# Optimization experiments

Measured on AMD Instinct MI355X. Metric: run time of the kernel, lower is better.

Reference implementation:

```python
import jax, jax.numpy as jnp
import numpy as np
import math

B, L, D = 4, 4096, 1024
PI = math.pi
LN_EPS = 1e-5


def setup_inputs() -> dict:
    key = jax.random.key(0)
    ks = jax.random.split(key, 16)
    s = 1.0 / math.sqrt(D)
    inp = {
        "x": jax.random.normal(ks[0], (B, L, D), dtype=jnp.float32),
        # Linear weights stored as [in, out] (torch W.T)
        "Wk": jax.random.normal(ks[1], (D, D), dtype=jnp.float32) * s,
        "bk": jnp.zeros((D,), dtype=jnp.float32),
        "Wq": jax.random.normal(ks[2], (D, D), dtype=jnp.float32) * s,
        "bq": jnp.zeros((D,), dtype=jnp.float32),
        "Wv": jax.random.normal(ks[3], (D, D), dtype=jnp.float32) * s,
        "bv": jnp.zeros((D,), dtype=jnp.float32),
        "ln_g": jnp.ones((D,), dtype=jnp.float32),
        "ln_b": jnp.zeros((D,), dtype=jnp.float32),
        "Wo": jax.random.normal(ks[4], (D, D), dtype=jnp.float32) * s,
        "bo": jnp.zeros((D,), dtype=jnp.float32),
        "Wg1": jax.random.normal(ks[5], (D, D // 4), dtype=jnp.float32) * s,
        "bg1": jnp.zeros((D // 4,), dtype=jnp.float32),
        "Wg2": jax.random.normal(ks[6], (D // 4, 1), dtype=jnp.float32) * (2.0 / math.sqrt(D)),
        "bg2": jnp.zeros((1,), dtype=jnp.float32),
        "pos_phases": jax.random.normal(ks[7], (L, D), dtype=jnp.float32) * PI,
    }
    return inp


def _layernorm(x, g, b):
    mu = jnp.mean(x, axis=-1, keepdims=True)
    var = jnp.var(x, axis=-1, keepdims=True)
    return (x - mu) * jax.lax.rsqrt(var + LN_EPS) * g + b


def reference(x, Wk, bk, Wq, bq, Wv, bv, ln_g, ln_b, Wo, bo, Wg1, bg1, Wg2, bg2, pos_phases):
    # dropout is identity in eval mode
    key_phases = jnp.tanh(x @ Wk + bk) * PI          # [B,L,D]
    query_phases = jnp.tanh(x @ Wq + bq) * PI        # [B,L,D]
    V = x @ Wv + bv                                   # [B,L,D]

    cos_k, sin_k = jnp.cos(key_phases), jnp.sin(key_phases)
    cos_q, sin_q = jnp.cos(query_phases), jnp.sin(query_phases)

    mem_real = jnp.cumsum(V * cos_k, axis=1)
    mem_imag = jnp.cumsum(V * sin_k, axis=1)
    content_retrieved = mem_real * cos_q + mem_imag * sin_q

    pp = pos_phases[: x.shape[1]]                     # [L,D]
    cos_p, sin_p = jnp.cos(pp), jnp.sin(pp)
    pos_mem_real = jnp.cumsum(V * cos_p, axis=1)
    pos_mem_imag = jnp.cumsum(V * sin_p, axis=1)
    pos_retrieved = pos_mem_real * cos_p + pos_mem_imag * sin_p

    gate = jax.nn.sigmoid(jax.nn.gelu(x @ Wg1 + bg1) @ Wg2 + bg2)  # [B,L,1]
    combined = gate * content_retrieved + (1.0 - gate) * pos_retrieved

    positions = jnp.arange(1, x.shape[1] + 1, dtype=jnp.float32)
    norm = jnp.sqrt(positions)[None, :, None]
    out = _layernorm(combined / norm, ln_g, ln_b) @ Wo + bo
    return x + out
```

## Files before the change

### kernel.cpp

```cpp
#include <hip/hip_runtime.h>
#include <math.h>

#define B_ 4
#define L_ 4096
#define D_ 1024
#define DG_ 256
#define NC_ 128
#define CL_ 32
#define PI_F 3.14159265358979323846f
#define LN_EPS_F 1e-5f

typedef __attribute__((ext_vector_type(8))) _Float16 f16x8;
typedef __attribute__((ext_vector_type(8))) short s16x8;
typedef __attribute__((ext_vector_type(4))) short s16x4;
typedef __attribute__((ext_vector_type(4))) float f32x4;

__device__ inline short f2h(float f) { return __builtin_bit_cast(short, (_Float16)f); }
__device__ inline float h2f(short s) { return (float)__builtin_bit_cast(_Float16, s); }

__device__ inline float ftanh(float x) {
    float e = __expf(2.0f * x);
    return 1.0f - 2.0f / (e + 1.0f);
}
__device__ inline void fsincos(float x, float* s, float* c) {
    *s = __sinf(x); *c = __cosf(x);
}

__device__ inline void gld16(const void* g, void* l) {
    __builtin_amdgcn_global_load_lds(
        (const __attribute__((address_space(1))) unsigned int*)g,
        (__attribute__((address_space(3))) unsigned int*)l, 16, 0, 0);
}

__global__ __launch_bounds__(256)
void conv_x(const float* __restrict__ x, short* __restrict__ xh, int n8)
{
    int t = blockIdx.x * 256 + threadIdx.x;
    if (t >= n8) return;
    const float4* p = (const float4*)x + (size_t)t * 2;
    float4 a = p[0], b = p[1];
    s16x8 v;
    v[0] = f2h(a.x); v[1] = f2h(a.y); v[2] = f2h(a.z); v[3] = f2h(a.w);
    v[4] = f2h(b.x); v[5] = f2h(b.y); v[6] = f2h(b.z); v[7] = f2h(b.w);
    *(s16x8*)(xh + (size_t)t * 8) = v;
}

__global__ __launch_bounds__(256)
void convT(const float* __restrict__ W, short* __restrict__ Th, int N)
{
    __shared__ float tile[64][65];
    const int n0 = blockIdx.x * 64, k0 = blockIdx.y * 64;
    const int t = threadIdx.x;
    const int r = t >> 4, c4 = (t & 15) * 4;

    #pragma unroll
    for (int i = 0; i < 4; ++i) {
        float4 v = *(const float4*)&W[(size_t)(k0 + r + i * 16) * N + n0 + c4];
        tile[r + i * 16][c4 + 0] = v.x;
        tile[r + i * 16][c4 + 1] = v.y;
        tile[r + i * 16][c4 + 2] = v.z;
        tile[r + i * 16][c4 + 3] = v.w;
    }
    __syncthreads();
    #pragma unroll
    for (int i = 0; i < 4; ++i) {
        const int n = r + i * 16;
        s16x4 o;
        o[0] = f2h(tile[c4 + 0][n]);
        o[1] = f2h(tile[c4 + 1][n]);
        o[2] = f2h(tile[c4 + 2][n]);
        o[3] = f2h(tile[c4 + 3][n]);
        *(s16x4*)&Th[(size_t)(n0 + n) * 1024 + k0 + c4] = o;
    }
}

#define SBAR() __builtin_amdgcn_sched_barrier(0)
#define BARRIER() do { SBAR(); __builtin_amdgcn_s_barrier(); SBAR(); } while (0)
#define PRIO1() __builtin_amdgcn_s_setprio(1)
#define PRIO0() __builtin_amdgcn_s_setprio(0)
#define LGKM0() do { asm volatile("s_waitcnt lgkmcnt(0)" ::: "memory"); \
                     __builtin_amdgcn_sched_barrier(0); } while (0)

#define DSR(dst, areg, OFS)                                              \
    asm volatile("ds_read_b128 %0, %1 offset:" OFS                       \
                 : "=v"(dst) : "v"(areg))

#define RDA4(areg)                                                       \
    DSR(af[0], areg, "0");    DSR(af[1], areg, "2048");                  \
    DSR(af[2], areg, "4096"); DSR(af[3], areg, "6144");
#define RDA4H(areg)                                                      \
    DSR(af[0], areg, "8192");  DSR(af[1], areg, "10240");                \
    DSR(af[2], areg, "12288"); DSR(af[3], areg, "14336");
#define RDB4(areg, KK)                                                   \
    DSR(bq[0][KK], areg, "0");    DSR(bq[1][KK], areg, "2048");          \
    DSR(bq[2][KK], areg, "4096"); DSR(bq[3][KK], areg, "6144");

#define MF(MG, KK)                                                       \
    _Pragma("unroll") for (int i_ = 0; i_ < 4; ++i_)                     \
    _Pragma("unroll") for (int n_ = 0; n_ < 4; ++n_)                     \
        acc[(MG)*4 + i_][n_] = __builtin_amdgcn_mfma_f32_16x16x32_f16(   \
            af[i_], bq[n_][KK], acc[(MG)*4 + i_][n_], 0, 0, 0);

template<int EPI, typename OT>
__global__ __launch_bounds__(512, 2)
void mgemm256(const short* __restrict__ A, const short* __restrict__ Bt,
              const float* __restrict__ X, OT* __restrict__ out0,
              short* __restrict__ out1, short* __restrict__ out2,
              const float* __restrict__ b0, const float* __restrict__ b1,
              const float* __restrict__ b2, const float* __restrict__ bg1p,
              const float* __restrict__ wg2p, float* __restrict__ gatep,
              int M, int N, int K)
{
    extern __shared__ char lds[];

    const int tid = threadIdx.x;
    const int w = tid >> 6, l = tid & 63;
    const int wr = w >> 2, wc = w & 3;
    const int fr = l & 15, kb = l >> 4;
    const int bm = blockIdx.x * 256, bn = blockIdx.y * 256;
    const int np = K >> 7;

    const int s = fr & 7;
    const int cK0 = (((s >> 2) & 1) << 6) | (((kb ^ s) & 3) << 4);
    const int aA0 = (wr << 14) + fr * 128 + cK0;
    const int aA1 = aA0 ^ 64;
    const int aB0 = 32768 + ((wc >> 1) << 14) + ((wc & 1) * 64 + fr) * 128 + cK0;
    const int aB1 = aB0 ^ 64;
    const int aA0o = aA0 + 65536, aA1o = aA1 + 65536;
    const int aB0o = aB0 + 65536, aB1o = aB1 + 65536;

    const int p0 = tid * 16;
    const int sr = p0 >> 7;
    const int sc = (p0 & 127) ^ ((sr & 7) << 4);
    const short* gA = A  + (size_t)(bm + sr) * K + (sc >> 1);
    const short* gB = Bt + (size_t)(bn + sr) * K + (sc >> 1);
    char* ldst = lds + (w << 10);
    const size_t q1 = (size_t)64 * K, q2 = 2 * q1, q3 = 3 * q1;

    f32x4 acc[8][4] = {};
    f16x8 af[4];
    f16x8 bq[4][2];

    gld16(gA,      ldst);          gld16(gA + q1, ldst + 8192);
    gld16(gA + q2, ldst + 16384);  gld16(gA + q3, ldst + 24576);
    gld16(gB,      ldst + 32768);  gld16(gB + q1, ldst + 40960);
    gld16(gB + q2, ldst + 49152);  gld16(gB + q3, ldst + 57344);
    gld16(gA +      64, ldst + 65536);
    gld16(gA + q2 + 64, ldst + 65536 + 16384);
    asm volatile("s_waitcnt vmcnt(2)" ::: "memory");
    BARRIER();

    const short* gAn = gA + 64;
    const short* gBn = gB + 64;

    for (int pp = 0; pp < np; ++pp) {
        const bool nl = (pp + 1 < np);

        RDA4(aA0); RDB4(aB0, 0);
        gld16(gBn,      ldst + 98304);
        gld16(gBn + q1, ldst + 98304 + 8192);
        BARRIER();
        LGKM0();
        PRIO1(); MF(0, 0); PRIO0();
        BARRIER();
        RDA4(aA1); RDB4(aB1, 1);
        gld16(gBn + q2, ldst + 98304 + 16384);
        gld16(gBn + q3, ldst + 98304 + 24576);
        BARRIER();
        LGKM0();
        PRIO1(); MF(0, 1); PRIO0();
        BARRIER();
        RDA4H(aA0);
        gld16(gAn + q1, ldst + 65536 + 8192);
        gld16(gAn + q3, ldst + 65536 + 24576);
        BARRIER();
        LGKM0();
        PRIO1(); MF(1, 0); PRIO0();
        BARRIER();
        RDA4H(aA1);
        if (nl) { gld16(gAn + 64, ldst); gld16(gAn + 64 + q2, ldst + 16384); }
        BARRIER();
        LGKM0();
        PRIO1(); MF(1, 1); PRIO0();
        SBAR();
        asm volatile("s_waitcnt vmcnt(2)" ::: "memory");
        __builtin_amdgcn_s_barrier(); SBAR();

        RDA4(aA0o); RDB4(aB0o, 0);
        if (nl) {
            gld16(gBn +      64, ldst + 32768);
            gld16(gBn + q1 + 64, ldst + 40960);
        }
        BARRIER();
        LGKM0();
        PRIO1(); MF(0, 0); PRIO0();
        BARRIER();
        RDA4(aA1o); RDB4(aB1o, 1);
        if (nl) {
            gld16(gBn + q2 + 64, ldst + 49152);
            gld16(gBn + q3 + 64, ldst + 57344);
        }
        BARRIER();
        LGKM0();
        PRIO1(); MF(0, 1); PRIO0();
        BARRIER();
        if (!nl) asm volatile("s_waitcnt vmcnt(0)" ::: "memory");
        RDA4H(aA0o);
        if (nl) {
            gld16(gAn + q1 + 64, ldst + 8192);
            gld16(gAn + q3 + 64, ldst + 24576);
        }
        BARRIER();
        LGKM0();
        PRIO1(); MF(1, 0); PRIO0();
        BARRIER();
        RDA4H(aA1o);
        if (nl) { gld16(gAn + 128, ldst + 65536); gld16(gAn + 128 + q2, ldst + 65536 + 16384); }
        BARRIER();
        LGKM0();
        PRIO1(); MF(1, 1); PRIO0();
        SBAR();
        if (nl) {
            asm volatile("s_waitcnt vmcnt(2)" ::: "memory");
            __builtin_amdgcn_s_barrier(); SBAR();
        }
        gAn += 128; gBn += 128;
    }

    if constexpr (EPI == 4) {
        if (bn < 3072) {
            short* op; const float* bp; bool dt;
            if (bn < 1024)      { op = (short*)out0; bp = b0; dt = true;  }
            else if (bn < 2048) { op = out1;         bp = b1; dt = true;  }
            else                { op = out2;         bp = b2; dt = false; }
            const int cb = bn & 1023;
            float bc[4];
            #pragma unroll
            for (int nf = 0; nf < 4; ++nf) bc[nf] = bp[cb + wc * 64 + nf * 16 + fr];
            #pragma unroll
            for (int mf = 0; mf < 8; ++mf)
                #pragma unroll
                for (int rr = 0; rr < 4; ++rr) {
                    const int row = bm + wr * 128 + mf * 16 + kb * 4 + rr;
                    #pragma unroll
                    for (int nf = 0; nf < 4; ++nf) {
                        const int cc = cb + wc * 64 + nf * 16 + fr;
                        float c = acc[mf][nf][rr] + bc[nf];
                        if (dt) c = ftanh(c) * PI_F;
                        op[(size_t)row * 1024 + cc] = f2h(c);
                    }
                }
        } else {
            float bg[4], wg[4];
            #pragma unroll
            for (int nf = 0; nf < 4; ++nf) {
                const int cl = wc * 64 + nf * 16 + fr;
                bg[nf] = bg1p[cl];
                wg[nf] = wg2p[cl];
            }
            #pragma unroll
            for (int mf = 0; mf < 8; ++mf)
                #pragma unroll
                for (int rr = 0; rr < 4; ++rr) {
                    const int row = bm + wr * 128 + mf * 16 + kb * 4 + rr;
                    float part = 0.f;
                    #pragma unroll
                    for (int nf = 0; nf < 4; ++nf) {
                        float c = acc[mf][nf][rr] + bg[nf];
                        float tt = 0.7978845608028654f * (c + 0.044715f * c * c * c);
                        float g = 0.5f * c * (1.0f + ftanh(tt));
                        part += g * wg[nf];
                    }
                    part += __shfl_xor(part, 1);
                    part += __shfl_xor(part, 2);
                    part += __shfl_xor(part, 4);
                    part += __shfl_xor(part, 8);
                    if (fr == 0) atomicAdd(&gatep[row], part);
                }
        }
    } else {
        float bc[4];
        #pragma unroll
        for (int nf = 0; nf < 4; ++nf) bc[nf] = b0[bn + wc * 64 + nf * 16 + fr];
        #pragma unroll
        for (int mf = 0; mf < 8; ++mf)
            #pragma unroll
            for (int rr = 0; rr < 4; ++rr) {
                const int row = bm + wr * 128 + mf * 16 + kb * 4 + rr;
                #pragma unroll
                for (int nf = 0; nf < 4; ++nf) {
                    const int col = bn + wc * 64 + nf * 16 + fr;
                    float c = acc[mf][nf][rr] + bc[nf] + X[(size_t)row * N + col];
                    ((float*)out0)[(size_t)row * N + col] = c;
                }
            }
    }
}

__global__ __launch_bounds__(256)
void passA(const short* __restrict__ V, const short* __restrict__ KP,
           const float* __restrict__ PP, f32x4* __restrict__ SI)
{
    const int bid = blockIdx.x;
    const int b = bid >> 7, c = bid & 127;
    const int d0 = threadIdx.x * 4;

    f32x4 cr = {}, ci = {}, pr = {}, pi = {};
    const size_t base  = ((size_t)b * L_ + (size_t)c * CL_) * D_ + d0;
    const size_t pbase = (size_t)c * CL_ * D_ + d0;
    for (int ll = 0; ll < CL_; ++ll) {
        s16x4 v4  = *(const s16x4*)&V [base + (size_t)ll * D_];
        s16x4 kp4 = *(const s16x4*)&KP[base + (size_t)ll * D_];
        f32x4 pp4 = *(const f32x4*)&PP[pbase + (size_t)ll * D_];
        #pragma unroll
        for (int j = 0; j < 4; ++j) {
            float v = h2f(v4[j]);
            float sk, ck, sp, cp;
            fsincos(h2f(kp4[j]), &sk, &ck);
            fsincos(pp4[j], &sp, &cp);
            cr[j] += v * ck; ci[j] += v * sk;
            pr[j] += v * cp; pi[j] += v * sp;
        }
    }
    const size_t sidx = ((size_t)bid << 10) + d0;
    #pragma unroll
    for (int j = 0; j < 4; ++j) {
        f32x4 o = { cr[j], ci[j], pr[j], pi[j] };
        SI[sidx + j] = o;
    }
}

__global__ __launch_bounds__(256)
void passB(f32x4* __restrict__ SI)
{
    const int t = blockIdx.x * 256 + threadIdx.x;
    const int b = t >> 10, d = t & 1023;
    f32x4 run = {};
    for (int c = 0; c < NC_; ++c) {
        const size_t idx = ((size_t)(b * NC_ + c) << 10) + d;
        f32x4 v = SI[idx];
        SI[idx] = run;
        run += v;
    }
}

__global__ __launch_bounds__(256)
void passC(const short* __restrict__ V, const short* KP,
           const short* __restrict__ QP, const float* __restrict__ PP,
           const float* __restrict__ gatep, const float* __restrict__ bg2,
           const f32x4* __restrict__ SI, const float* __restrict__ ln_g,
           const float* __restrict__ ln_b, short* Yb)
{
    const int bid = blockIdx.x;
    const int b = bid >> 7, c = bid & 127;
    const int d0 = threadIdx.x * 4;

    const size_t sidx = ((size_t)bid << 10) + d0;
    f32x4 cr, ci, pr, pi;
    #pragma unroll
    for (int j = 0; j < 4; ++j) {
        f32x4 s = SI[sidx + j];
        cr[j] = s[0]; ci[j] = s[1]; pr[j] = s[2]; pi[j] = s[3];
    }
    const f32x4 g_ln = *(const f32x4*)&ln_g[d0];
    const f32x4 b_ln = *(const f32x4*)&ln_b[d0];
    const float bg2v = bg2[0];

    __shared__ float2 lred[2][4];
    const int wid = threadIdx.x >> 6;
    const int lane = threadIdx.x & 63;

    for (int l0 = 0; l0 < CL_; ++l0) {
        const int ll = c * CL_ + l0;
        const size_t off = ((size_t)b * L_ + ll) * D_ + d0;
        s16x4 v4  = *(const s16x4*)&V [off];
        s16x4 kp4 = *(const s16x4*)&KP[off];
        s16x4 qp4 = *(const s16x4*)&QP[off];
        f32x4 pp4 = *(const f32x4*)&PP[(size_t)ll * D_ + d0];
        const float gv = 1.0f / (1.0f + __expf(-(gatep[b * L_ + ll] + bg2v)));
        const float rs_pos = rsqrtf((float)(ll + 1));

        f32x4 u;
        #pragma unroll
        for (int j = 0; j < 4; ++j) {
            float v = h2f(v4[j]);
            float sk, ck, sq, cq, sp, cp;
            fsincos(h2f(kp4[j]), &sk, &ck);
            fsincos(h2f(qp4[j]), &sq, &cq);
            fsincos(pp4[j], &sp, &cp);
            cr[j] += v * ck; ci[j] += v * sk;
            pr[j] += v * cp; pi[j] += v * sp;
            float content = cr[j] * cq + ci[j] * sq;
            float posr    = pr[j] * cp + pi[j] * sp;
            u[j] = (gv * content + (1.0f - gv) * posr) * rs_pos;
        }

        float s  = u[0] + u[1] + u[2] + u[3];
        float s2 = u[0]*u[0] + u[1]*u[1] + u[2]*u[2] + u[3]*u[3];
        #pragma unroll
        for (int o = 32; o; o >>= 1) {
            s  += __shfl_down(s, o);
            s2 += __shfl_down(s2, o);
        }
        const int pb = l0 & 1;
        if (lane == 0) lred[pb][wid] = make_float2(s, s2);
        __syncthreads();
        float ts  = lred[pb][0].x + lred[pb][1].x + lred[pb][2].x + lred[pb][3].x;
        float ts2 = lred[pb][0].y + lred[pb][1].y + lred[pb][2].y + lred[pb][3].y;
        const float mu  = ts * (1.0f / D_);
        const float var = ts2 * (1.0f / D_) - mu * mu;
        const float rsv = rsqrtf(var + LN_EPS_F);
        s16x4 yo;
        #pragma unroll
        for (int j = 0; j < 4; ++j)
            yo[j] = f2h((u[j] - mu) * rsv * g_ln[j] + b_ln[j]);
        *(s16x4*)&Yb[off] = yo;
    }
}

extern "C" void kernel_launch(void* const* d_in, const int* in_sizes, int n_in,
                              void* d_out, int out_size, void* d_ws, size_t ws_size,
                              hipStream_t stream)
{
    const float* x    = (const float*)d_in[0];
    const float* Wk   = (const float*)d_in[1];
    const float* bk   = (const float*)d_in[2];
    const float* Wq   = (const float*)d_in[3];
    const float* bq   = (const float*)d_in[4];
    const float* Wv   = (const float*)d_in[5];
    const float* bv   = (const float*)d_in[6];
    const float* ln_g = (const float*)d_in[7];
    const float* ln_b = (const float*)d_in[8];
    const float* Wo   = (const float*)d_in[9];
    const float* bo   = (const float*)d_in[10];
    const float* Wg1  = (const float*)d_in[11];
    const float* bg1  = (const float*)d_in[12];
    const float* Wg2  = (const float*)d_in[13];
    const float* bg2  = (const float*)d_in[14];
    const float* PP   = (const float*)d_in[15];

    float* out = (float*)d_out;

    const size_t BLD   = (size_t)B_ * L_ * D_;
    const size_t SZ_X  = BLD * 2;
    const size_t SZ_R1 = (size_t)B_ * L_ * DG_ * 2;
    const size_t SZ_GT = (size_t)B_ * L_ * 4;
    const size_t NEED  = SZ_X + SZ_R1 + 3 * SZ_X + SZ_GT;
    if (ws_size < NEED) {
        hipMemcpyAsync(d_out, d_in[0], BLD * sizeof(float),
                       hipMemcpyDeviceToDevice, stream);
        return;
    }

    char* wsb = (char*)d_ws;
    short* xh   = (short*)(wsb);
    char*  r1   = wsb + SZ_X;
    short* Wcat = (short*)r1;
    short* KP   = (short*)(r1 + SZ_R1);
    short* QP   = (short*)((char*)KP + SZ_X);
    short* V    = (short*)((char*)QP + SZ_X);
    float* gatep = (float*)((char*)V + SZ_X);
    short* WtO  = (short*)(wsb);
    f32x4* SI   = (f32x4*)(wsb + 2097152);
    short* Yb   = KP;

    const int M = B_ * L_;
    dim3 blk(256);

    conv_x<<<(int)(BLD / 8 / 256), blk, 0, stream>>>(x, xh, (int)(BLD / 8));
    dim3 gT(D_ / 64, 16);
    dim3 gTg(DG_ / 64, 16);
    convT<<<gT, blk, 0, stream>>>(Wk, Wcat + (size_t)0 * D_ * D_, D_);
    convT<<<gT, blk, 0, stream>>>(Wq, Wcat + (size_t)1 * D_ * D_, D_);
    convT<<<gT, blk, 0, stream>>>(Wv, Wcat + (size_t)2 * D_ * D_, D_);
    convT<<<gTg, blk, 0, stream>>>(Wg1, Wcat + (size_t)3 * D_ * D_, DG_);

    hipMemsetAsync(gatep, 0, SZ_GT, stream);
    dim3 gQKV(M / 256, 3328 / 256);
    hipLaunchKernelGGL((mgemm256<4, short>), gQKV, dim3(512), 131072, stream,
                       xh, Wcat, nullptr, KP, QP, V, bk, bq, bv,
                       bg1, Wg2, gatep, M, 3328, D_);

    convT<<<gT, blk, 0, stream>>>(Wo, WtO, D_);

    passA<<<B_ * NC_, blk, 0, stream>>>(V, KP, PP, SI);
    passB<<<(B_ * D_) / 256, blk, 0, stream>>>(SI);
    passC<<<B_ * NC_, blk, 0, stream>>>(V, KP, QP, PP, gatep, bg2, SI,
                                        ln_g, ln_b, Yb);

    dim3 gO(M / 256, D_ / 256);
    hipLaunchKernelGGL((mgemm256<3, float>), gO, dim3(512), 131072, stream,
                       Yb, WtO, x, out, nullptr, nullptr, bo, nullptr, nullptr,
                       nullptr, nullptr, nullptr, M, D_, D_);
}
```

Baseline: 309.2 us.

## Replace 256x256 GEMM with 128x128 tile kernel and split gate GEMM

Swaps the 8-wave 256x256-tile GEMM for a 4-wave 128x128-tile kernel. It uses a simpler double-buffered LDS pipeline with fewer barriers and half the LDS per block. The gate projection (Wg1) moves out of the fused QKV launch into its own GEMM with a dedicated epilogue. That requires a separate transposed Wg1 buffer in the workspace. The smaller tiles give more blocks and occupancy but lower data reuse per block, and they add an extra kernel launch.

```diff
diff --git a/kernel.cpp b/kernel.cpp
--- a/kernel.cpp
+++ b/kernel.cpp
@@ -85,208 +85,165 @@
     asm volatile("ds_read_b128 %0, %1 offset:" OFS                       \
                  : "=v"(dst) : "v"(areg))
 
-#define RDA4(areg)                                                       \
+#define RDAF(areg)                                                       \
     DSR(af[0], areg, "0");    DSR(af[1], areg, "2048");                  \
     DSR(af[2], areg, "4096"); DSR(af[3], areg, "6144");
-#define RDA4H(areg)                                                      \
-    DSR(af[0], areg, "8192");  DSR(af[1], areg, "10240");                \
-    DSR(af[2], areg, "12288"); DSR(af[3], areg, "14336");
-#define RDB4(areg, KK)                                                   \
-    DSR(bq[0][KK], areg, "0");    DSR(bq[1][KK], areg, "2048");          \
-    DSR(bq[2][KK], areg, "4096"); DSR(bq[3][KK], areg, "6144");
-
-#define MF(MG, KK)                                                       \
+#define RDBF(areg)                                                       \
+    DSR(bq[0], areg, "0");    DSR(bq[1], areg, "2048");                  \
+    DSR(bq[2], areg, "4096"); DSR(bq[3], areg, "6144");
+
+#define MF16()                                                           \
     _Pragma("unroll") for (int i_ = 0; i_ < 4; ++i_)                     \
     _Pragma("unroll") for (int n_ = 0; n_ < 4; ++n_)                     \
-        acc[(MG)*4 + i_][n_] = __builtin_amdgcn_mfma_f32_16x16x32_f16(   \
-            af[i_], bq[n_][KK], acc[(MG)*4 + i_][n_], 0, 0, 0);
+        acc[i_][n_] = __builtin_amdgcn_mfma_f32_16x16x32_f16(            \
+            af[i_], bq[n_], acc[i_][n_], 0, 0, 0);
 
 template<int EPI, typename OT>
-__global__ __launch_bounds__(512, 2)
-void mgemm256(const short* __restrict__ A, const short* __restrict__ Bt,
-              const float* __restrict__ X, OT* __restrict__ out0,
-              short* __restrict__ out1, short* __restrict__ out2,
-              const float* __restrict__ b0, const float* __restrict__ b1,
-              const float* __restrict__ b2, const float* __restrict__ bg1p,
-              const float* __restrict__ wg2p, float* __restrict__ gatep,
-              int M, int N, int K)
+__global__ __launch_bounds__(256, 2)
+void gemm128(const short* __restrict__ A, const short* __restrict__ Bt,
+             const float* __restrict__ X, OT* __restrict__ out0,
+             short* __restrict__ out1, short* __restrict__ out2,
+             const float* __restrict__ b0, const float* __restrict__ b1,
+             const float* __restrict__ b2, const float* __restrict__ wg2p,
+             float* __restrict__ gatep, int M, int N, int K)
 {
     extern __shared__ char lds[];
 
     const int tid = threadIdx.x;
     const int w = tid >> 6, l = tid & 63;
-    const int wr = w >> 2, wc = w & 3;
+    const int wr = w >> 1, wc = w & 1;
     const int fr = l & 15, kb = l >> 4;
-    const int bm = blockIdx.x * 256, bn = blockIdx.y * 256;
-    const int np = K >> 7;
+    const int bm = blockIdx.x * 128, bn = blockIdx.y * 128;
 
     const int s = fr & 7;
     const int cK0 = (((s >> 2) & 1) << 6) | (((kb ^ s) & 3) << 4);
-    const int aA0 = (wr << 14) + fr * 128 + cK0;
-    const int aA1 = aA0 ^ 64;
-    const int aB0 = 32768 + ((wc >> 1) << 14) + ((wc & 1) * 64 + fr) * 128 + cK0;
-    const int aB1 = aB0 ^ 64;
-    const int aA0o = aA0 + 65536, aA1o = aA1 + 65536;
-    const int aB0o = aB0 + 65536, aB1o = aB1 + 65536;
-
-    const int p0 = tid * 16;
-    const int sr = p0 >> 7;
-    const int sc = (p0 & 127) ^ ((sr & 7) << 4);
+    const int aA0e = (wr * 64 + fr) * 128 + cK0;
+    const int aA1e = aA0e ^ 64;
+    const int aB0e = 16384 + (wc * 64 + fr) * 128 + cK0;
+    const int aB1e = aB0e ^ 64;
+    const int aA0o = aA0e + 32768, aA1o = aA1e + 32768;
+    const int aB0o = aB0e + 32768, aB1o = aB1e + 32768;
+
+    const int p16 = tid * 16;
+    const int sr = p16 >> 7;
+    const int scb = p16 & 127;
+    const int sc = scb ^ ((sr & 7) << 4);
     const short* gA = A  + (size_t)(bm + sr) * K + (sc >> 1);
     const short* gB = Bt + (size_t)(bn + sr) * K + (sc >> 1);
-    char* ldst = lds + (w << 10);
-    const size_t q1 = (size_t)64 * K, q2 = 2 * q1, q3 = 3 * q1;
-
-    f32x4 acc[8][4] = {};
-    f16x8 af[4];
-    f16x8 bq[4][2];
-
-    gld16(gA,      ldst);          gld16(gA + q1, ldst + 8192);
-    gld16(gA + q2, ldst + 16384);  gld16(gA + q3, ldst + 24576);
-    gld16(gB,      ldst + 32768);  gld16(gB + q1, ldst + 40960);
-    gld16(gB + q2, ldst + 49152);  gld16(gB + q3, ldst + 57344);
-    gld16(gA +      64, ldst + 65536);
-    gld16(gA + q2 + 64, ldst + 65536 + 16384);
-    asm volatile("s_waitcnt vmcnt(2)" ::: "memory");
+    char* ldA = lds + (w << 10);
+    const size_t r32 = (size_t)32 * K;
+
+    f32x4 acc[4][4] = {};
+    f16x8 af[4], bq[4];
+
+    #pragma unroll
+    for (int i = 0; i < 4; ++i) gld16(gA + i * r32, ldA + i * 4096);
+    #pragma unroll
+    for (int i = 0; i < 4; ++i) gld16(gB + i * r32, ldA + 16384 + i * 4096);
+    asm volatile("s_waitcnt vmcnt(0)" ::: "memory");
     BARRIER();
 
-    const short* gAn = gA + 64;
-    const short* gBn = gB + 64;
+    const short* gAt = gA;
+    const short* gBt = gB;
+    const int np = K >> 7;
 
     for (int pp = 0; pp < np; ++pp) {
         const bool nl = (pp + 1 < np);
 
-        RDA4(aA0); RDB4(aB0, 0);
-        gld16(gBn,      ldst + 98304);
-        gld16(gBn + q1, ldst + 98304 + 8192);
-        BARRIER();
+        RDAF(aA0e); RDBF(aB0e);
+        #pragma unroll
+        for (int i = 0; i < 4; ++i) gld16(gAt + 64 + i * r32, ldA + 32768 + i * 4096);
         LGKM0();
-        PRIO1(); MF(0, 0); PRIO0();
-        BARRIER();
-        RDA4(aA1); RDB4(aB1, 1);
-        gld16(gBn + q2, ldst + 98304 + 16384);
-        gld16(gBn + q3, ldst + 98304 + 24576);
-        BARRIER();
+        PRIO1(); MF16(); PRIO0();
+        RDAF(aA1e); RDBF(aB1e);
+        #pragma unroll
+        for (int i = 0; i < 4; ++i) gld16(gBt + 64 + i * r32, ldA + 49152 + i * 4096);
         LGKM0();
-        PRIO1(); MF(0, 1); PRIO0();
-        BARRIER();
-        RDA4H(aA0);
-        gld16(gAn + q1, ldst + 65536 + 8192);
-        gld16(gAn + q3, ldst + 65536 + 24576);
-        BARRIER();
+        PRIO1(); MF16(); PRIO0();
+        SBAR();
+        asm volatile("s_waitcnt vmcnt(0)" ::: "memory");
+        __builtin_amdgcn_s_barrier(); SBAR();
+
+        RDAF(aA0o); RDBF(aB0o);
+        if (nl) {
+            #pragma unroll
+            for (int i = 0; i < 4; ++i) gld16(gAt + 128 + i * r32, ldA + i * 4096);
+        }
         LGKM0();
-        PRIO1(); MF(1, 0); PRIO0();
-        BARRIER();
-        RDA4H(aA1);
-        if (nl) { gld16(gAn + 64, ldst); gld16(gAn + 64 + q2, ldst + 16384); }
-        BARRIER();
+        PRIO1(); MF16(); PRIO0();
+        RDAF(aA1o); RDBF(aB1o);
+        if (nl) {
+            #pragma unroll
+            for (int i = 0; i < 4; ++i) gld16(gBt + 128 + i * r32, ldA + 16384 + i * 4096);
+        }
         LGKM0();
-        PRIO1(); MF(1, 1); PRIO0();
-        SBAR();
-        asm volatile("s_waitcnt vmcnt(2)" ::: "memory");
-        __builtin_amdgcn_s_barrier(); SBAR();
-
-        RDA4(aA0o); RDB4(aB0o, 0);
-        if (nl) {
-            gld16(gBn +      64, ldst + 32768);
-            gld16(gBn + q1 + 64, ldst + 40960);
-        }
-        BARRIER();
-        LGKM0();
-        PRIO1(); MF(0, 0); PRIO0();
-        BARRIER();
-        RDA4(aA1o); RDB4(aB1o, 1);
-        if (nl) {
-            gld16(gBn + q2 + 64, ldst + 49152);
-            gld16(gBn + q3 + 64, ldst + 57344);
-        }
-        BARRIER();
-        LGKM0();
-        PRIO1(); MF(0, 1); PRIO0();
-        BARRIER();
-        if (!nl) asm volatile("s_waitcnt vmcnt(0)" ::: "memory");
-        RDA4H(aA0o);
-        if (nl) {
-            gld16(gAn + q1 + 64, ldst + 8192);
-            gld16(gAn + q3 + 64, ldst + 24576);
-        }
-        BARRIER();
-        LGKM0();
-        PRIO1(); MF(1, 0); PRIO0();
-        BARRIER();
-        RDA4H(aA1o);
-        if (nl) { gld16(gAn + 128, ldst + 65536); gld16(gAn + 128 + q2, ldst + 65536 + 16384); }
-        BARRIER();
-        LGKM0();
-        PRIO1(); MF(1, 1); PRIO0();
+        PRIO1(); MF16(); PRIO0();
         SBAR();
         if (nl) {
-            asm volatile("s_waitcnt vmcnt(2)" ::: "memory");
+            asm volatile("s_waitcnt vmcnt(0)" ::: "memory");
             __builtin_amdgcn_s_barrier(); SBAR();
         }
-        gAn += 128; gBn += 128;
+        gAt += 128; gBt += 128;
     }
 
     if constexpr (EPI == 4) {
-        if (bn < 3072) {
-            short* op; const float* bp; bool dt;
-            if (bn < 1024)      { op = (short*)out0; bp = b0; dt = true;  }
-            else if (bn < 2048) { op = out1;         bp = b1; dt = true;  }
-            else                { op = out2;         bp = b2; dt = false; }
-            const int cb = bn & 1023;
-            float bc[4];
+        short* op; const float* bp; bool dt;
+        if (bn < 1024)      { op = (short*)out0; bp = b0; dt = true;  }
+        else if (bn < 2048) { op = out1;         bp = b1; dt = true;  }
+        else                { op = out2;         bp = b2; dt = false; }
+        const int cb = bn & 1023;
+        float bc[4];
+        #pragma unroll
+        for (int nf = 0; nf < 4; ++nf) bc[nf] = bp[cb + wc * 64 + nf * 16 + fr];
+        #pragma unroll
+        for (int mf = 0; mf < 4; ++mf)
             #pragma unroll
-            for (int nf = 0; nf < 4; ++nf) bc[nf] = bp[cb + wc * 64 + nf * 16 + fr];
+            for (int rr = 0; rr < 4; ++rr) {
+                const int row = bm + wr * 64 + mf * 16 + kb * 4 + rr;
+                #pragma unroll
+                for (int nf = 0; nf < 4; ++nf) {
+                    const int cc = cb + wc * 64 + nf * 16 + fr;
+                    float c = acc[mf][nf][rr] + bc[nf];
+                    if (dt) c = ftanh(c) * PI_F;
+                    op[(size_t)row * 1024 + cc] = f2h(c);
+                }
+            }
+    } else if constexpr (EPI == 5) {
+        float bg[4], wg[4];
+        #pragma unroll
+        for (int nf = 0; nf < 4; ++nf) {
+            const int cl = bn + wc * 64 + nf * 16 + fr;
+            bg[nf] = b0[cl];
+            wg[nf] = wg2p[cl];
+        }
+        #pragma unroll
+        for (int mf = 0; mf < 4; ++mf)
             #pragma unroll
-            for (int mf = 0; mf < 8; ++mf)
+            for (int rr = 0; rr < 4; ++rr) {
+                const int row = bm + wr * 64 + mf * 16 + kb * 4 + rr;
+                float part = 0.f;
                 #pragma unroll
-                for (int rr = 0; rr < 4; ++rr) {
-                    const int row = bm + wr * 128 + mf * 16 + kb * 4 + rr;
-                    #pragma unroll
-                    for (int nf = 0; nf < 4; ++nf) {
-                        const int cc = cb + wc * 64 + nf * 16 + fr;
-                        float c = acc[mf][nf][rr] + bc[nf];
-                        if (dt) c = ftanh(c) * PI_F;
-                        op[(size_t)row * 1024 + cc] = f2h(c);
-                    }
+                for (int nf = 0; nf < 4; ++nf) {
+                    float c = acc[mf][nf][rr] + bg[nf];
+                    float tt = 0.7978845608028654f * (c + 0.044715f * c * c * c);
+                    float g = 0.5f * c * (1.0f + ftanh(tt));
+                    part += g * wg[nf];
                 }
-        } else {
-            float bg[4], wg[4];
-            #pragma unroll
-            for (int nf = 0; nf < 4; ++nf) {
-                const int cl = wc * 64 + nf * 16 + fr;
-                bg[nf] = bg1p[cl];
-                wg[nf] = wg2p[cl];
+                part += __shfl_xor(part, 1);
+                part += __shfl_xor(part, 2);
+                part += __shfl_xor(part, 4);
+                part += __shfl_xor(part, 8);
+                if (fr == 0) atomicAdd(&gatep[row], part);
             }
-            #pragma unroll
-            for (int mf = 0; mf < 8; ++mf)
-                #pragma unroll
-                for (int rr = 0; rr < 4; ++rr) {
-                    const int row = bm + wr * 128 + mf * 16 + kb * 4 + rr;
-                    float part = 0.f;
-                    #pragma unroll
-                    for (int nf = 0; nf < 4; ++nf) {
-                        float c = acc[mf][nf][rr] + bg[nf];
-                        float tt = 0.7978845608028654f * (c + 0.044715f * c * c * c);
-                        float g = 0.5f * c * (1.0f + ftanh(tt));
-                        part += g * wg[nf];
-                    }
-                    part += __shfl_xor(part, 1);
-                    part += __shfl_xor(part, 2);
-                    part += __shfl_xor(part, 4);
-                    part += __shfl_xor(part, 8);
-                    if (fr == 0) atomicAdd(&gatep[row], part);
-                }
-        }
     } else {
         float bc[4];
         #pragma unroll
         for (int nf = 0; nf < 4; ++nf) bc[nf] = b0[bn + wc * 64 + nf * 16 + fr];
         #pragma unroll
-        for (int mf = 0; mf < 8; ++mf)
+        for (int mf = 0; mf < 4; ++mf)
             #pragma unroll
             for (int rr = 0; rr < 4; ++rr) {
-                const int row = bm + wr * 128 + mf * 16 + kb * 4 + rr;
+                const int row = bm + wr * 64 + mf * 16 + kb * 4 + rr;
                 #pragma unroll
                 for (int nf = 0; nf < 4; ++nf) {
                     const int col = bn + wc * 64 + nf * 16 + fr;
@@ -444,8 +401,9 @@
     const size_t BLD   = (size_t)B_ * L_ * D_;
     const size_t SZ_X  = BLD * 2;
     const size_t SZ_R1 = (size_t)B_ * L_ * DG_ * 2;
+    const size_t SZ_G1 = (size_t)D_ * DG_ * 2;
     const size_t SZ_GT = (size_t)B_ * L_ * 4;
-    const size_t NEED  = SZ_X + SZ_R1 + 3 * SZ_X + SZ_GT;
+    const size_t NEED  = SZ_X + SZ_R1 + SZ_G1 + 3 * SZ_X + SZ_GT;
     if (ws_size < NEED) {
         hipMemcpyAsync(d_out, d_in[0], BLD * sizeof(float),
                        hipMemcpyDeviceToDevice, stream);
@@ -456,7 +414,8 @@
     short* xh   = (short*)(wsb);
     char*  r1   = wsb + SZ_X;
     short* Wcat = (short*)r1;
-    short* KP   = (short*)(r1 + SZ_R1);
+    short* Wg1T = (short*)(r1 + SZ_R1);
+    short* KP   = (short*)(r1 + SZ_R1 + SZ_G1);
     short* QP   = (short*)((char*)KP + SZ_X);
     short* V    = (short*)((char*)QP + SZ_X);
     float* gatep = (float*)((char*)V + SZ_X);
@@ -473,13 +432,17 @@
     convT<<<gT, blk, 0, stream>>>(Wk, Wcat + (size_t)0 * D_ * D_, D_);
     convT<<<gT, blk, 0, stream>>>(Wq, Wcat + (size_t)1 * D_ * D_, D_);
     convT<<<gT, blk, 0, stream>>>(Wv, Wcat + (size_t)2 * D_ * D_, D_);
-    convT<<<gTg, blk, 0, stream>>>(Wg1, Wcat + (size_t)3 * D_ * D_, DG_);
-
+    convT<<<gTg, blk, 0, stream>>>(Wg1, Wg1T, DG_);
     hipMemsetAsync(gatep, 0, SZ_GT, stream);
-    dim3 gQKV(M / 256, 3328 / 256);
-    hipLaunchKernelGGL((mgemm256<4, short>), gQKV, dim3(512), 131072, stream,
+
+    dim3 gQKV(M / 128, 3072 / 128);
+    hipLaunchKernelGGL((gemm128<4, short>), gQKV, blk, 65536, stream,
                        xh, Wcat, nullptr, KP, QP, V, bk, bq, bv,
-                       bg1, Wg2, gatep, M, 3328, D_);
+                       nullptr, nullptr, M, 3072, D_);
+    dim3 gH(M / 128, DG_ / 128);
+    hipLaunchKernelGGL((gemm128<5, short>), gH, blk, 65536, stream,
+                       xh, Wg1T, nullptr, nullptr, nullptr, nullptr,
+                       bg1, nullptr, nullptr, Wg2, gatep, M, DG_, D_);
 
     convT<<<gT, blk, 0, stream>>>(Wo, WtO, D_);
 
@@ -488,8 +451,8 @@
     passC<<<B_ * NC_, blk, 0, stream>>>(V, KP, QP, PP, gatep, bg2, SI,
                                         ln_g, ln_b, Yb);
 
-    dim3 gO(M / 256, D_ / 256);
-    hipLaunchKernelGGL((mgemm256<3, float>), gO, dim3(512), 131072, stream,
+    dim3 gO(M / 128, D_ / 128);
+    hipLaunchKernelGGL((gemm128<3, float>), gO, blk, 65536, stream,
                        Yb, WtO, x, out, nullptr, nullptr, bo, nullptr, nullptr,
-                       nullptr, nullptr, nullptr, M, D_, D_);
-}
+                       nullptr, nullptr, M, D_, D_);
+}
```

Measured after the change: 306.5 us. About the same (-0.9%).

## Split gate projection into separate 128-tile GEMM and drop sched barriers

Applied to the files above, without the earlier changes.

The gate-hidden projection (x@Wg1, 256 columns) is taken out of the fused QKV 256x256 GEMM, so that GEMM now covers exactly 3072 columns with no partial column tile. The gate path moves to a new 128x128-tile, 256-thread GEMM kernel with its own GELU/Wg2 reduction epilogue and atomic accumulation. Separately, the sched_barrier wrappers around s_barrier are removed, which lets the compiler reorder code around the barriers. The trade is an extra kernel launch and a second read of x for the gate GEMM, in exchange for a cleaner tile grid and a more uniform QKV epilogue.

```diff
diff --git a/kernel.cpp b/kernel.cpp
--- a/kernel.cpp
+++ b/kernel.cpp
@@ -74,12 +74,12 @@
     }
 }
 
-#define SBAR() __builtin_amdgcn_sched_barrier(0)
-#define BARRIER() do { SBAR(); __builtin_amdgcn_s_barrier(); SBAR(); } while (0)
+#define BARRIER() __builtin_amdgcn_s_barrier()
 #define PRIO1() __builtin_amdgcn_s_setprio(1)
 #define PRIO0() __builtin_amdgcn_s_setprio(0)
 #define LGKM0() do { asm volatile("s_waitcnt lgkmcnt(0)" ::: "memory"); \
                      __builtin_amdgcn_sched_barrier(0); } while (0)
+#define VMC(N) asm volatile("s_waitcnt vmcnt(" #N ")" ::: "memory")
 
 #define DSR(dst, areg, OFS)                                              \
     asm volatile("ds_read_b128 %0, %1 offset:" OFS                       \
@@ -107,9 +107,7 @@
               const float* __restrict__ X, OT* __restrict__ out0,
               short* __restrict__ out1, short* __restrict__ out2,
               const float* __restrict__ b0, const float* __restrict__ b1,
-              const float* __restrict__ b2, const float* __restrict__ bg1p,
-              const float* __restrict__ wg2p, float* __restrict__ gatep,
-              int M, int N, int K)
+              const float* __restrict__ b2, int M, int N, int K)
 {
     extern __shared__ char lds[];
 
@@ -147,7 +145,7 @@
     gld16(gB + q2, ldst + 49152);  gld16(gB + q3, ldst + 57344);
     gld16(gA +      64, ldst + 65536);
     gld16(gA + q2 + 64, ldst + 65536 + 16384);
-    asm volatile("s_waitcnt vmcnt(2)" ::: "memory");
+    VMC(2);
     BARRIER();
 
     const short* gAn = gA + 64;
@@ -163,6 +161,7 @@
         LGKM0();
         PRIO1(); MF(0, 0); PRIO0();
         BARRIER();
+
         RDA4(aA1); RDB4(aB1, 1);
         gld16(gBn + q2, ldst + 98304 + 16384);
         gld16(gBn + q3, ldst + 98304 + 24576);
@@ -170,6 +169,7 @@
         LGKM0();
         PRIO1(); MF(0, 1); PRIO0();
         BARRIER();
+
         RDA4H(aA0);
         gld16(gAn + q1, ldst + 65536 + 8192);
         gld16(gAn + q3, ldst + 65536 + 24576);
@@ -177,14 +177,14 @@
         LGKM0();
         PRIO1(); MF(1, 0); PRIO0();
         BARRIER();
+
         RDA4H(aA1);
         if (nl) { gld16(gAn + 64, ldst); gld16(gAn + 64 + q2, ldst + 16384); }
         BARRIER();
         LGKM0();
         PRIO1(); MF(1, 1); PRIO0();
-        SBAR();
-        asm volatile("s_waitcnt vmcnt(2)" ::: "memory");
-        __builtin_amdgcn_s_barrier(); SBAR();
+        VMC(2);
+        BARRIER();
 
         RDA4(aA0o); RDB4(aB0o, 0);
         if (nl) {
@@ -195,6 +195,7 @@
         LGKM0();
         PRIO1(); MF(0, 0); PRIO0();
         BARRIER();
+
         RDA4(aA1o); RDB4(aB1o, 1);
         if (nl) {
             gld16(gBn + q2 + 64, ldst + 49152);
@@ -204,7 +205,8 @@
         LGKM0();
         PRIO1(); MF(0, 1); PRIO0();
         BARRIER();
-        if (!nl) asm volatile("s_waitcnt vmcnt(0)" ::: "memory");
+
+        if (!nl) VMC(0);
         RDA4H(aA0o);
         if (nl) {
             gld16(gAn + q1 + 64, ldst + 8192);
@@ -214,70 +216,41 @@
         LGKM0();
         PRIO1(); MF(1, 0); PRIO0();
         BARRIER();
+
         RDA4H(aA1o);
         if (nl) { gld16(gAn + 128, ldst + 65536); gld16(gAn + 128 + q2, ldst + 65536 + 16384); }
         BARRIER();
         LGKM0();
         PRIO1(); MF(1, 1); PRIO0();
-        SBAR();
-        if (nl) {
-            asm volatile("s_waitcnt vmcnt(2)" ::: "memory");
-            __builtin_amdgcn_s_barrier(); SBAR();
+        if (nl) {
+            VMC(2);
+            BARRIER();
         }
         gAn += 128; gBn += 128;
     }
 
     if constexpr (EPI == 4) {
-        if (bn < 3072) {
-            short* op; const float* bp; bool dt;
-            if (bn < 1024)      { op = (short*)out0; bp = b0; dt = true;  }
-            else if (bn < 2048) { op = out1;         bp = b1; dt = true;  }
-            else                { op = out2;         bp = b2; dt = false; }
-            const int cb = bn & 1023;
-            float bc[4];
+        short* op; const float* bp; bool dt;
+        if (bn < 1024)      { op = (short*)out0; bp = b0; dt = true;  }
+        else if (bn < 2048) { op = out1;         bp = b1; dt = true;  }
+        else                { op = out2;         bp = b2; dt = false; }
+        const int cb = bn & 1023;
+        float bc[4];
+        #pragma unroll
+        for (int nf = 0; nf < 4; ++nf) bc[nf] = bp[cb + wc * 64 + nf * 16 + fr];
+        #pragma unroll
+        for (int mf = 0; mf < 8; ++mf)
             #pragma unroll
-            for (int nf = 0; nf < 4; ++nf) bc[nf] = bp[cb + wc * 64 + nf * 16 + fr];
-            #pragma unroll
-            for (int mf = 0; mf < 8; ++mf)
+            for (int rr = 0; rr < 4; ++rr) {
+                const int row = bm + wr * 128 + mf * 16 + kb * 4 + rr;
                 #pragma unroll
-                for (int rr = 0; rr < 4; ++rr) {
-                    const int row = bm + wr * 128 + mf * 16 + kb * 4 + rr;
-                    #pragma unroll
-                    for (int nf = 0; nf < 4; ++nf) {
-                        const int cc = cb + wc * 64 + nf * 16 + fr;
-                        float c = acc[mf][nf][rr] + bc[nf];
-                        if (dt) c = ftanh(c) * PI_F;
-                        op[(size_t)row * 1024 + cc] = f2h(c);
-                    }
+                for (int nf = 0; nf < 4; ++nf) {
+                    const int cc = cb + wc * 64 + nf * 16 + fr;
+                    float c = acc[mf][nf][rr] + bc[nf];
+                    if (dt) c = ftanh(c) * PI_F;
+                    op[(size_t)row * 1024 + cc] = f2h(c);
                 }
-        } else {
-            float bg[4], wg[4];
-            #pragma unroll
-            for (int nf = 0; nf < 4; ++nf) {
-                const int cl = wc * 64 + nf * 16 + fr;
-                bg[nf] = bg1p[cl];
-                wg[nf] = wg2p[cl];
             }
-            #pragma unroll
-            for (int mf = 0; mf < 8; ++mf)
-                #pragma unroll
-                for (int rr = 0; rr < 4; ++rr) {
-                    const int row = bm + wr * 128 + mf * 16 + kb * 4 + rr;
-                    float part = 0.f;
-                    #pragma unroll
-                    for (int nf = 0; nf < 4; ++nf) {
-                        float c = acc[mf][nf][rr] + bg[nf];
-                        float tt = 0.7978845608028654f * (c + 0.044715f * c * c * c);
-                        float g = 0.5f * c * (1.0f + ftanh(tt));
-                        part += g * wg[nf];
-                    }
-                    part += __shfl_xor(part, 1);
-                    part += __shfl_xor(part, 2);
-                    part += __shfl_xor(part, 4);
-                    part += __shfl_xor(part, 8);
-                    if (fr == 0) atomicAdd(&gatep[row], part);
-                }
-        }
     } else {
         float bc[4];
         #pragma unroll
@@ -295,6 +268,129 @@
                 }
             }
     }
+}
+
+#define RDAF(areg)                                                       \
+    DSR(af[0], areg, "0");    DSR(af[1], areg, "2048");                  \
+    DSR(af[2], areg, "4096"); DSR(af[3], areg, "6144");
+#define RDBF(areg)                                                       \
+    DSR(bqs[0], areg, "0");    DSR(bqs[1], areg, "2048");                \
+    DSR(bqs[2], areg, "4096"); DSR(bqs[3], areg, "6144");
+
+#define MF16()                                                           \
+    _Pragma("unroll") for (int i_ = 0; i_ < 4; ++i_)                     \
+    _Pragma("unroll") for (int n_ = 0; n_ < 4; ++n_)                     \
+        acc[i_][n_] = __builtin_amdgcn_mfma_f32_16x16x32_f16(            \
+            af[i_], bqs[n_], acc[i_][n_], 0, 0, 0);
+
+template<int EPI>
+__global__ __launch_bounds__(256, 2)
+void gemm128(const short* __restrict__ A, const short* __restrict__ Bt,
+             const float* __restrict__ b0, const float* __restrict__ wg2p,
+             float* __restrict__ gatep, int M, int N, int K)
+{
+    extern __shared__ char lds[];
+
+    const int tid = threadIdx.x;
+    const int w = tid >> 6, l = tid & 63;
+    const int wr = w >> 1, wc = w & 1;
+    const int fr = l & 15, kb = l >> 4;
+    const int bm = blockIdx.x * 128, bn = blockIdx.y * 128;
+
+    const int s = fr & 7;
+    const int cK0 = (((s >> 2) & 1) << 6) | (((kb ^ s) & 3) << 4);
+    const int aA0e = (wr * 64 + fr) * 128 + cK0;
+    const int aA1e = aA0e ^ 64;
+    const int aB0e = 16384 + (wc * 64 + fr) * 128 + cK0;
+    const int aB1e = aB0e ^ 64;
+    const int aA0o = aA0e + 32768, aA1o = aA1e + 32768;
+    const int aB0o = aB0e + 32768, aB1o = aB1e + 32768;
+
+    const int p16 = tid * 16;
+    const int sr = p16 >> 7;
+    const int sc = (p16 & 127) ^ ((sr & 7) << 4);
+    const short* gA = A  + (size_t)(bm + sr) * K + (sc >> 1);
+    const short* gB = Bt + (size_t)(bn + sr) * K + (sc >> 1);
+    char* ldA = lds + (w << 10);
+    const size_t r32 = (size_t)32 * K;
+
+    f32x4 acc[4][4] = {};
+    f16x8 af[4], bqs[4];
+
+    #pragma unroll
+    for (int i = 0; i < 4; ++i) gld16(gA + i * r32, ldA + i * 4096);
+    #pragma unroll
+    for (int i = 0; i < 4; ++i) gld16(gB + i * r32, ldA + 16384 + i * 4096);
+    VMC(0);
+    BARRIER();
+
+    const short* gAt = gA;
+    const short* gBt = gB;
+    const int np = K >> 7;
+
+    for (int pp = 0; pp < np; ++pp) {
+        const bool nl = (pp + 1 < np);
+
+        RDAF(aA0e); RDBF(aB0e);
+        #pragma unroll
+        for (int i = 0; i < 4; ++i) gld16(gAt + 64 + i * r32, ldA + 32768 + i * 4096);
+        LGKM0();
+        PRIO1(); MF16(); PRIO0();
+        RDAF(aA1e); RDBF(aB1e);
+        #pragma unroll
+        for (int i = 0; i < 4; ++i) gld16(gBt + 64 + i * r32, ldA + 49152 + i * 4096);
+        LGKM0();
+        PRIO1(); MF16(); PRIO0();
+        VMC(0);
+        BARRIER();
+
+        RDAF(aA0o); RDBF(aB0o);
+        if (nl) {
+            #pragma unroll
+            for (int i = 0; i < 4; ++i) gld16(gAt + 128 + i * r32, ldA + i * 4096);
+        }
+        LGKM0();
+        PRIO1(); MF16(); PRIO0();
+        RDAF(aA1o); RDBF(aB1o);
+        if (nl) {
+            #pragma unroll
+            for (int i = 0; i < 4; ++i) gld16(gBt + 128 + i * r32, ldA + 16384 + i * 4096);
+        }
+        LGKM0();
+        PRIO1(); MF16(); PRIO0();
+        if (nl) {
+            VMC(0);
+            BARRIER();
+        }
+        gAt += 128; gBt += 128;
+    }
+
+    float bg[4], wg[4];
+    #pragma unroll
+    for (int nf = 0; nf < 4; ++nf) {
+        const int cl = bn + wc * 64 + nf * 16 + fr;
+        bg[nf] = b0[cl];
+        wg[nf] = wg2p[cl];
+    }
+    #pragma unroll
+    for (int mf = 0; mf < 4; ++mf)
+        #pragma unroll
+        for (int rr = 0; rr < 4; ++rr) {
+            const int row = bm + wr * 64 + mf * 16 + kb * 4 + rr;
+            float part = 0.f;
+            #pragma unroll
+            for (int nf = 0; nf < 4; ++nf) {
+                float c = acc[mf][nf][rr] + bg[nf];
+                float tt = 0.7978845608028654f * (c + 0.044715f * c * c * c);
+                float g = 0.5f * c * (1.0f + ftanh(tt));
+                part += g * wg[nf];
+            }
+            part += __shfl_xor(part, 1);
+            part += __shfl_xor(part, 2);
+            part += __shfl_xor(part, 4);
+            part += __shfl_xor(part, 8);
+            if (fr == 0) atomicAdd(&gatep[row], part);
+        }
 }
 
 __global__ __launch_bounds__(256)
@@ -444,8 +540,9 @@
     const size_t BLD   = (size_t)B_ * L_ * D_;
     const size_t SZ_X  = BLD * 2;
     const size_t SZ_R1 = (size_t)B_ * L_ * DG_ * 2;
+    const size_t SZ_G1 = (size_t)D_ * DG_ * 2;
     const size_t SZ_GT = (size_t)B_ * L_ * 4;
-    const size_t NEED  = SZ_X + SZ_R1 + 3 * SZ_X + SZ_GT;
+    const size_t NEED  = SZ_X + SZ_R1 + SZ_G1 + 3 * SZ_X + SZ_GT;
     if (ws_size < NEED) {
         hipMemcpyAsync(d_out, d_in[0], BLD * sizeof(float),
                        hipMemcpyDeviceToDevice, stream);
@@ -456,7 +553,8 @@
     short* xh   = (short*)(wsb);
     char*  r1   = wsb + SZ_X;
     short* Wcat = (short*)r1;
-    short* KP   = (short*)(r1 + SZ_R1);
+    short* Wg1T = (short*)(r1 + SZ_R1);
+    short* KP   = (short*)(r1 + SZ_R1 + SZ_G1);
     short* QP   = (short*)((char*)KP + SZ_X);
     short* V    = (short*)((char*)QP + SZ_X);
     float* gatep = (float*)((char*)V + SZ_X);
@@ -473,13 +571,15 @@
     convT<<<gT, blk, 0, stream>>>(Wk, Wcat + (size_t)0 * D_ * D_, D_);
     convT<<<gT, blk, 0, stream>>>(Wq, Wcat + (size_t)1 * D_ * D_, D_);
     convT<<<gT, blk, 0, stream>>>(Wv, Wcat + (size_t)2 * D_ * D_, D_);
-    convT<<<gTg, blk, 0, stream>>>(Wg1, Wcat + (size_t)3 * D_ * D_, DG_);
-
+    convT<<<gTg, blk, 0, stream>>>(Wg1, Wg1T, DG_);
     hipMemsetAsync(gatep, 0, SZ_GT, stream);
-    dim3 gQKV(M / 256, 3328 / 256);
+
+    dim3 gQKV(M / 256, 3072 / 256);
     hipLaunchKernelGGL((mgemm256<4, short>), gQKV, dim3(512), 131072, stream,
-                       xh, Wcat, nullptr, KP, QP, V, bk, bq, bv,
-                       bg1, Wg2, gatep, M, 3328, D_);
+                       xh, Wcat, nullptr, KP, QP, V, bk, bq, bv, M, 3072, D_);
+    dim3 gH(M / 128, DG_ / 128);
+    hipLaunchKernelGGL((gemm128<5>), gH, blk, 65536, stream,
+                       xh, Wg1T, bg1, Wg2, gatep, M, DG_, D_);
 
     convT<<<gT, blk, 0, stream>>>(Wo, WtO, D_);
 
@@ -491,5 +591,5 @@
     dim3 gO(M / 256, D_ / 256);
     hipLaunchKernelGGL((mgemm256<3, float>), gO, dim3(512), 131072, stream,
                        Yb, WtO, x, out, nullptr, nullptr, bo, nullptr, nullptr,
-                       nullptr, nullptr, nullptr, M, D_, D_);
-}
+                       M, D_, D_);
+}
```

Measured after the change: 291.5 us. 5.7% less time.
